# Kernel optimization log

Measured on AMD Instinct MI355X. Metric: run time of the kernel, lower is better.

## Reference

```python
import jax, jax.numpy as jnp
import numpy as np

B, N, NI, H, NO = 4, 262144, 4, 64, 3  # batch, pixels, inputs, hidden width, outputs


def setup_inputs() -> dict:
    key = jax.random.key(0)
    k = jax.random.split(key, 7)
    return {
        "x": jax.random.normal(k[0], (B, N, NI), dtype=jnp.float32),
        "W1": jax.random.normal(k[1], (NI, H), dtype=jnp.float32),
        "b1": jax.random.normal(k[2], (H,), dtype=jnp.float32),
        "W2": jax.random.normal(k[3], (H, H), dtype=jnp.float32),
        "b2": jax.random.normal(k[4], (H,), dtype=jnp.float32),
        "W3": jax.random.normal(k[5], (H, NO), dtype=jnp.float32),
        "b3": jax.random.normal(k[6], (NO,), dtype=jnp.float32),
    }


def reference(x, W1, b1, W2, b2, W3, b3):
    # Layered message passing over a fully connected CPPN genome:
    # each hidden node sums weighted incoming states, adds bias, applies tanh.
    h1 = jnp.tanh(jnp.einsum("bni,ih->bnh", x, W1) + b1)   # hidden layer 1 states [B,N,H]
    h2 = jnp.tanh(jnp.einsum("bnh,hk->bnk", h1, W2) + b2)  # hidden layer 2 states [B,N,H]
    out = jnp.einsum("bnh,ho->bno", h2, W3) + b3           # output nodes: identity activation, bias only
    out = jnp.moveaxis(out, -1, 0)                         # channel_first=True -> [NO, B, N]
    out = (out - out.min()) / (out.max() - out.min())      # global min-max normalization
    return jnp.clip(out, 0.0, 1.0)
```

## Files before the change

### kernel.cpp

```cpp
#include <hip/hip_runtime.h>
#include <math.h>

#define NPIX 1048576
#define HH 64
#define NO 3
#define NBLK 2048
#define ITER 8
#define NOUT4 786432
#define K2C 2.8853900817779268f

typedef float f32x4 __attribute__((ext_vector_type(4)));
typedef __bf16 bf16x8 __attribute__((ext_vector_type(8)));
typedef __bf16 bf16x2 __attribute__((ext_vector_type(2)));

union BF8 { __bf16 h[8]; bf16x8 v; uint4 u4; };
union PK2 { bf16x2 h; unsigned u; };
union F4U { float f[4]; uint4 u; f32x4 v; };

#define MFMA16(a, b, c) __builtin_amdgcn_mfma_f32_16x16x32_bf16((a), (b), (c), 0, 0, 0)

__device__ __forceinline__ int hsel(int k) {
    const int G = (k & 31) >> 3, j = k & 7;
    return ((k >= 32) ? 32 : 0) + ((j >= 4) ? 16 : 0) + 4 * G + (j & 3);
}

__device__ __forceinline__ void tanh4_pack(const f32x4 c, unsigned* lo, unsigned* hi) {
    const float a0 = __builtin_amdgcn_exp2f(c[0]) + 1.0f;
    const float a1 = __builtin_amdgcn_exp2f(c[1]) + 1.0f;
    const float a2 = __builtin_amdgcn_exp2f(c[2]) + 1.0f;
    const float a3 = __builtin_amdgcn_exp2f(c[3]) + 1.0f;
    const float r01 = __builtin_amdgcn_rcpf(a0 * a1);
    const float r23 = __builtin_amdgcn_rcpf(a2 * a3);
    const float t0 = fmaf(-2.0f, a1 * r01, 1.0f);
    const float t1 = fmaf(-2.0f, a0 * r01, 1.0f);
    const float t2 = fmaf(-2.0f, a3 * r23, 1.0f);
    const float t3 = fmaf(-2.0f, a2 * r23, 1.0f);
    PK2 L, H;
    L.h = bf16x2{(__bf16)t0, (__bf16)t1};
    H.h = bf16x2{(__bf16)t2, (__bf16)t3};
    *lo = L.u; *hi = H.u;
}

__global__ __launch_bounds__(256) void cppn_pack(
    const float* __restrict__ W1, const float* __restrict__ b1,
    const float* __restrict__ W2, const float* __restrict__ b2,
    const float* __restrict__ W3, const float* __restrict__ b3,
    uint4* __restrict__ fr)
{
    const int t = threadIdx.x, w = t >> 6, l = t & 63, g = l >> 4, q = l & 15;
    uint4* o = fr + l * 18;

    if (w == 0) {
        #pragma unroll
        for (int m = 0; m < 4; ++m) {
            BF8 tt;
            #pragma unroll
            for (int j = 0; j < 8; ++j) {
                const int k = g * 8 + j;
                float v = 0.0f;
                if (k < 4) v = W1[k * HH + m * 16 + q];
                else if (k == 4) v = b1[m * 16 + q];
                tt.h[j] = (__bf16)(K2C * v);
            }
            o[m] = tt.u4;
        }
    } else if (w == 1 || w == 2) {
        const int s = w - 1;
        #pragma unroll
        for (int m = 0; m < 4; ++m) {
            BF8 tt;
            #pragma unroll
            for (int j = 0; j < 8; ++j)
                tt.h[j] = (__bf16)(K2C * W2[hsel(s * 32 + g * 8 + j) * HH + m * 16 + q]);
            o[4 + s * 4 + m] = tt.u4;
        }
    } else {
        #pragma unroll
        for (int s = 0; s < 2; ++s) {
            BF8 tt;
            #pragma unroll
            for (int j = 0; j < 8; ++j)
                tt.h[j] = (q < NO) ? (__bf16)W3[hsel(s * 32 + g * 8 + j) * NO + q] : (__bf16)0.0f;
            o[12 + s] = tt.u4;
        }
        #pragma unroll
        for (int m = 0; m < 4; ++m) {
            F4U tt;
            #pragma unroll
            for (int r = 0; r < 4; ++r) tt.f[r] = K2C * b2[m * 16 + g * 4 + r];
            o[14 + m] = tt.u;
        }
    }
}

__global__ __launch_bounds__(256) void cppn_main(
    const float* __restrict__ x,
    const float* __restrict__ b3,
    const uint4* __restrict__ fr,
    float* __restrict__ out,
    float* __restrict__ pmin, float* __restrict__ pmax)
{
    __shared__ float rmin[4], rmax[4];

    const int t = threadIdx.x;
    const int w = t >> 6;
    const int l = t & 63;
    const int g = l >> 4;
    const int q = l & 15;

    const uint4* fo = fr + l * 18;
    bf16x8 A1[4], A2[2][4], A3[2];
    #pragma unroll
    for (int m = 0; m < 4; ++m) { BF8 u; u.u4 = fo[m]; A1[m] = u.v; }
    #pragma unroll
    for (int s = 0; s < 2; ++s)
        #pragma unroll
        for (int m = 0; m < 4; ++m) { BF8 u; u.u4 = fo[4 + s * 4 + m]; A2[s][m] = u.v; }
    #pragma unroll
    for (int s = 0; s < 2; ++s) { BF8 u; u.u4 = fo[12 + s]; A3[s] = u.v; }
    f32x4 Ci2[4];
    #pragma unroll
    for (int m = 0; m < 4; ++m) { F4U u; u.u = fo[14 + m]; Ci2[m] = u.v; }
    const float b30 = b3[0], b31 = b3[1], b32 = b3[2];

    const f32x4 z = {0.0f, 0.0f, 0.0f, 0.0f};
    float vmin = INFINITY, vmax = -INFINITY;

    const int pbase = ((blockIdx.x * 4 + w) * ITER) * 16 + q;
    const float4* x4 = reinterpret_cast<const float4*>(x);

    float4 cur = x4[pbase];

    #pragma unroll 2
    for (int it = 0; it < ITER; ++it) {
        const int itn = (it + 1 < ITER) ? it + 1 : it;
        const float4 nxt = x4[pbase + itn * 16];

        BF8 bx;
        bx.u4 = uint4{0, 0, 0, 0};
        if (g == 0) {
            PK2 p01, p23;
            p01.h = bf16x2{(__bf16)cur.x, (__bf16)cur.y};
            p23.h = bf16x2{(__bf16)cur.z, (__bf16)cur.w};
            bx.u4.x = p01.u;
            bx.u4.y = p23.u;
            bx.u4.z = 0x3F80u;
        }

        f32x4 c1[4];
        #pragma unroll
        for (int m = 0; m < 4; ++m) c1[m] = MFMA16(A1[m], bx.v, z);

        unsigned pkx[4], pky[4];
        #pragma unroll
        for (int m = 0; m < 4; ++m) tanh4_pack(c1[m], &pkx[m], &pky[m]);
        BF8 Bf0, Bf1;
        Bf0.u4 = uint4{pkx[0], pky[0], pkx[1], pky[1]};
        Bf1.u4 = uint4{pkx[2], pky[2], pkx[3], pky[3]};

        f32x4 c2[4];
        #pragma unroll
        for (int m = 0; m < 4; ++m) {
            c2[m] = MFMA16(A2[0][m], Bf0.v, Ci2[m]);
            c2[m] = MFMA16(A2[1][m], Bf1.v, c2[m]);
        }
        #pragma unroll
        for (int m = 0; m < 4; ++m) tanh4_pack(c2[m], &pkx[m], &pky[m]);
        BF8 Bg0, Bg1;
        Bg0.u4 = uint4{pkx[0], pky[0], pkx[1], pky[1]};
        Bg1.u4 = uint4{pkx[2], pky[2], pkx[3], pky[3]};

        f32x4 c3 = MFMA16(A3[0], Bg0.v, z);
        c3 = MFMA16(A3[1], Bg1.v, c3);

        if (g == 0) {
            const int pxg = pbase + it * 16;
            const float o0 = c3[0] + b30;
            const float o1 = c3[1] + b31;
            const float o2 = c3[2] + b32;
            out[0 * NPIX + pxg] = o0;
            out[1 * NPIX + pxg] = o1;
            out[2 * NPIX + pxg] = o2;
            vmin = fminf(vmin, fminf(fminf(o0, o1), o2));
            vmax = fmaxf(vmax, fmaxf(fmaxf(o0, o1), o2));
        }
        cur = nxt;
    }

    #pragma unroll
    for (int off = 32; off > 0; off >>= 1) {
        vmin = fminf(vmin, __shfl_down(vmin, off));
        vmax = fmaxf(vmax, __shfl_down(vmax, off));
    }
    if (l == 0) { rmin[w] = vmin; rmax[w] = vmax; }
    __syncthreads();
    if (t == 0) {
        pmin[blockIdx.x] = fminf(fminf(rmin[0], rmin[1]), fminf(rmin[2], rmin[3]));
        pmax[blockIdx.x] = fmaxf(fmaxf(rmax[0], rmax[1]), fmaxf(rmax[2], rmax[3]));
    }
}

__global__ __launch_bounds__(256) void cppn_normred(
    float4* __restrict__ out,
    const float* __restrict__ pmin, const float* __restrict__ pmax)
{
    __shared__ float rmin[4], rmax[4];
    const int t = threadIdx.x, w = t >> 6, l = t & 63;
    float mn = INFINITY, mx = -INFINITY;
    #pragma unroll
    for (int i = 0; i < NBLK / 256; ++i) {
        mn = fminf(mn, pmin[i * 256 + t]);
        mx = fmaxf(mx, pmax[i * 256 + t]);
    }
    #pragma unroll
    for (int off = 32; off > 0; off >>= 1) {
        mn = fminf(mn, __shfl_down(mn, off));
        mx = fmaxf(mx, __shfl_down(mx, off));
    }
    if (l == 0) { rmin[w] = mn; rmax[w] = mx; }
    __syncthreads();
    mn = fminf(fminf(rmin[0], rmin[1]), fminf(rmin[2], rmin[3]));
    mx = fmaxf(fmaxf(rmax[0], rmax[1]), fmaxf(rmax[2], rmax[3]));
    const float inv = __fdividef(1.0f, mx - mn);

    const int i = blockIdx.x * 256 + t;
    float4 v = out[i];
    v.x = fminf(fmaxf((v.x - mn) * inv, 0.0f), 1.0f);
    v.y = fminf(fmaxf((v.y - mn) * inv, 0.0f), 1.0f);
    v.z = fminf(fmaxf((v.z - mn) * inv, 0.0f), 1.0f);
    v.w = fminf(fmaxf((v.w - mn) * inv, 0.0f), 1.0f);
    out[i] = v;
}

extern "C" void kernel_launch(void* const* d_in, const int* in_sizes, int n_in,
                              void* d_out, int out_size, void* d_ws, size_t ws_size,
                              hipStream_t stream) {
    const float* x  = (const float*)d_in[0];
    const float* W1 = (const float*)d_in[1];
    const float* b1 = (const float*)d_in[2];
    const float* W2 = (const float*)d_in[3];
    const float* b2 = (const float*)d_in[4];
    const float* W3 = (const float*)d_in[5];
    const float* b3 = (const float*)d_in[6];
    float* out = (float*)d_out;

    float* pmin = (float*)((char*)d_ws + 1024);
    float* pmax = (float*)((char*)d_ws + 1024 + 8192);
    uint4* fr   = (uint4*)((char*)d_ws + 32768);

    cppn_pack<<<1, 256, 0, stream>>>(W1, b1, W2, b2, W3, b3, fr);
    cppn_main<<<NBLK, 256, 0, stream>>>(x, b3, fr, out, pmin, pmax);
    cppn_normred<<<NOUT4 / 256, 256, 0, stream>>>((float4*)out, pmin, pmax);
}
```

Baseline: 52.97 us.

## Stage weight fragments in LDS and reload per iteration instead of registers

Measured after the change: 54.61 us. 1.03x slower.

```diff
diff --git a/kernel.cpp b/kernel.cpp
--- a/kernel.cpp
+++ b/kernel.cpp
@@ -8,6 +8,7 @@
 #define ITER 8
 #define NOUT4 786432
 #define K2C 2.8853900817779268f
+#define NFRAG 18
 
 typedef float f32x4 __attribute__((ext_vector_type(4)));
 typedef __bf16 bf16x8 __attribute__((ext_vector_type(8)));
@@ -48,7 +49,7 @@
     uint4* __restrict__ fr)
 {
     const int t = threadIdx.x, w = t >> 6, l = t & 63, g = l >> 4, q = l & 15;
-    uint4* o = fr + l * 18;
+    uint4* o = fr + l * NFRAG;
 
     if (w == 0) {
         #pragma unroll
@@ -100,6 +101,7 @@
     float* __restrict__ out,
     float* __restrict__ pmin, float* __restrict__ pmax)
 {
+    __shared__ uint4 sfr[NFRAG * 64];
     __shared__ float rmin[4], rmax[4];
 
     const int t = threadIdx.x;
@@ -108,31 +110,25 @@
     const int g = l >> 4;
     const int q = l & 15;
 
-    const uint4* fo = fr + l * 18;
-    bf16x8 A1[4], A2[2][4], A3[2];
-    #pragma unroll
-    for (int m = 0; m < 4; ++m) { BF8 u; u.u4 = fo[m]; A1[m] = u.v; }
-    #pragma unroll
-    for (int s = 0; s < 2; ++s)
-        #pragma unroll
-        for (int m = 0; m < 4; ++m) { BF8 u; u.u4 = fo[4 + s * 4 + m]; A2[s][m] = u.v; }
-    #pragma unroll
-    for (int s = 0; s < 2; ++s) { BF8 u; u.u4 = fo[12 + s]; A3[s] = u.v; }
-    f32x4 Ci2[4];
-    #pragma unroll
-    for (int m = 0; m < 4; ++m) { F4U u; u.u = fo[14 + m]; Ci2[m] = u.v; }
+    for (int i = t; i < NFRAG * 64; i += 256)
+        sfr[(i % NFRAG) * 64 + (i / NFRAG)] = fr[i];
+    __syncthreads();
+
     const float b30 = b3[0], b31 = b3[1], b32 = b3[2];
-
     const f32x4 z = {0.0f, 0.0f, 0.0f, 0.0f};
     float vmin = INFINITY, vmax = -INFINITY;
 
     const int pbase = ((blockIdx.x * 4 + w) * ITER) * 16 + q;
     const float4* x4 = reinterpret_cast<const float4*>(x);
-
     float4 cur = x4[pbase];
 
-    #pragma unroll 2
+    const char* const sb = (const char*)sfr;
+    int slo = l * 16;
+
     for (int it = 0; it < ITER; ++it) {
+        asm volatile("" : "+v"(slo));
+        const char* sp = sb + slo;
+
         const int itn = (it + 1 < ITER) ? it + 1 : it;
         const float4 nxt = x4[pbase + itn * 16];
 
@@ -149,7 +145,10 @@
 
         f32x4 c1[4];
         #pragma unroll
-        for (int m = 0; m < 4; ++m) c1[m] = MFMA16(A1[m], bx.v, z);
+        for (int m = 0; m < 4; ++m) {
+            BF8 a; a.u4 = *(const uint4*)(sp + m * 1024);
+            c1[m] = MFMA16(a.v, bx.v, z);
+        }
 
         unsigned pkx[4], pky[4];
         #pragma unroll
@@ -158,20 +157,35 @@
         Bf0.u4 = uint4{pkx[0], pky[0], pkx[1], pky[1]};
         Bf1.u4 = uint4{pkx[2], pky[2], pkx[3], pky[3]};
 
+        __builtin_amdgcn_sched_barrier(0);
+
         f32x4 c2[4];
         #pragma unroll
         for (int m = 0; m < 4; ++m) {
-            c2[m] = MFMA16(A2[0][m], Bf0.v, Ci2[m]);
-            c2[m] = MFMA16(A2[1][m], Bf1.v, c2[m]);
-        }
+            BF8 a; a.u4 = *(const uint4*)(sp + (4 + m) * 1024);
+            F4U ci; ci.u = *(const uint4*)(sp + (14 + m) * 1024);
+            c2[m] = MFMA16(a.v, Bf0.v, ci.v);
+        }
+        __builtin_amdgcn_sched_barrier(0);
+        #pragma unroll
+        for (int m = 0; m < 4; ++m) {
+            BF8 a; a.u4 = *(const uint4*)(sp + (8 + m) * 1024);
+            c2[m] = MFMA16(a.v, Bf1.v, c2[m]);
+        }
+
         #pragma unroll
         for (int m = 0; m < 4; ++m) tanh4_pack(c2[m], &pkx[m], &pky[m]);
         BF8 Bg0, Bg1;
         Bg0.u4 = uint4{pkx[0], pky[0], pkx[1], pky[1]};
         Bg1.u4 = uint4{pkx[2], pky[2], pkx[3], pky[3]};
 
-        f32x4 c3 = MFMA16(A3[0], Bg0.v, z);
-        c3 = MFMA16(A3[1], Bg1.v, c3);
+        __builtin_amdgcn_sched_barrier(0);
+
+        BF8 a30, a31;
+        a30.u4 = *(const uint4*)(sp + 12 * 1024);
+        a31.u4 = *(const uint4*)(sp + 13 * 1024);
+        f32x4 c3 = MFMA16(a30.v, Bg0.v, z);
+        c3 = MFMA16(a31.v, Bg1.v, c3);
 
         if (g == 0) {
             const int pxg = pbase + it * 16;
```
